# Kernel optimization log

Measured on AMD Instinct MI355X. Metric: run time of the kernel, lower is better.

## Reference

```python
import math
import jax, jax.numpy as jnp
import numpy as np

B, L, E, H, NL = 8, 512, 512, 8, 2


def setup_inputs() -> dict:
    key = jax.random.key(0)
    ks = jax.random.split(key, 12)
    s = 0.02  # weight init scale
    return {
        "inputs_4e": jax.random.normal(ks[0], (B, L, 4 * E), jnp.float32),
        "query_embed": jax.random.normal(ks[1], (B, L, E), jnp.float32),
        "rel": jax.random.normal(ks[2], (B, L, L), jnp.float32),
        "resp_rel": jax.random.normal(ks[3], (B, L, L), jnp.float32),
        "timestamp": jax.random.uniform(ks[4], (B, L, L), jnp.float32) * 10.0,
        "l1": jax.random.uniform(ks[5], (1,), jnp.float32),
        "l2": jax.random.uniform(ks[6], (1,), jnp.float32),
        "l3": jax.random.uniform(ks[7], (1,), jnp.float32),
        "Win": jax.random.normal(ks[8], (4 * E, E), jnp.float32) * s,
        "b_in": jnp.zeros((E,), jnp.float32),
        "Wqkv": jax.random.normal(ks[9], (NL, 3, E, E), jnp.float32) * s,
        "bqkv": jnp.zeros((NL, 3, E), jnp.float32),
        "Wf1": jax.random.normal(ks[10], (2 * E, E), jnp.float32) * s,
        "bf1": jnp.zeros((E,), jnp.float32),
        "Wf2": jax.random.normal(ks[11], (E, 1), jnp.float32) * s,
        "bf2": jnp.zeros((1,), jnp.float32),
    }


def _mha(q_in, k_in, v_in, Wq, bq, Wk, bk, Wv, bv,
         rel, resp_rel, timestamp, l1, l2, l3, mask):
    Bb, Ll, Ee = q_in.shape
    d = Ee // H

    def split(x, W, b):  # (B,L,E) -> (B,H,L,d)
        return (x @ W + b).reshape(Bb, Ll, H, d).transpose(0, 2, 1, 3)

    q = split(q_in, Wq, bq)
    k = split(k_in, Wk, bk)
    v = split(v_in, Wv, bv)

    # relation softmax: zero out where mask==False, -1e4 at zeros
    maskf = mask.astype(rel.dtype)              # (1,1,L,L)
    rel_m = rel[:, None, :, :] * maskf          # (B,1,L,L), broadcasts over heads
    rel_attn = jax.nn.softmax(jnp.where(rel_m == 0, -1e4, rel_m), axis=-1)
    resp_m = resp_rel[:, None, :, :] * maskf
    resp_attn = jax.nn.softmax(jnp.where(resp_m == 0, -1e4, resp_m), axis=-1)

    # QK softmax with causal mask
    scores = jnp.einsum('bhqd,bhkd->bhqk', q, k) / math.sqrt(d)
    scores = jnp.where(mask, -1e9, scores)
    prob_attn = jax.nn.softmax(scores, axis=-1)

    # time-decay softmax
    ts = jnp.exp(-jnp.abs(timestamp))[:, None, :, :]  # (B,1,L,L)
    ts = jnp.where(mask, -jnp.inf, ts)
    time_attn = jax.nn.softmax(ts, axis=-1)

    # blend (ablation flags all True)
    p = (1.0 - l2) * prob_attn + l2 * time_attn
    p = (1.0 - l1) * p + l1 * rel_attn
    p = (1.0 - l3) * p + l3 * resp_attn

    out = jnp.einsum('bhqk,bhkd->bhqd', p, v)
    out = out.transpose(0, 2, 1, 3).reshape(Bb, Ll, Ee)
    return out, p


def reference(inputs_4e, query_embed, rel, resp_rel, timestamp,
              l1, l2, l3, Win, b_in, Wqkv, bqkv, Wf1, bf1, Wf2, bf2):
    mask = jnp.triu(jnp.ones((1, 1, L, L), dtype=bool), k=1)  # future mask
    inputs = jax.nn.relu(inputs_4e @ Win + b_in)              # lin_in_interaction

    outputs, attn = _mha(query_embed, inputs, inputs,
                         Wqkv[0, 0], bqkv[0, 0], Wqkv[0, 1], bqkv[0, 1],
                         Wqkv[0, 2], bqkv[0, 2],
                         rel, resp_rel, timestamp, l1, l2, l3, mask)
    for i in range(1, NL):
        residual, attn = _mha(query_embed, outputs, outputs,
                              Wqkv[i, 0], bqkv[i, 0], Wqkv[i, 1], bqkv[i, 1],
                              Wqkv[i, 2], bqkv[i, 2],
                              rel, resp_rel, timestamp, l1, l2, l3, mask)
        outputs = outputs + jax.nn.relu(residual)

    concat_q = jnp.concatenate([outputs, query_embed], axis=-1)  # (B,L,2E)
    h = jax.nn.relu(concat_q @ Wf1 + bf1)
    return h @ Wf2 + bf2  # (B,L,1)
```

## Files before the change

kernel.cpp:

```cpp
#include <hip/hip_runtime.h>
#include <math.h>

namespace {
constexpr int B = 8, L = 512, E = 512, H = 8;
constexpr int M = B * L;
}

typedef float f32x4 __attribute__((ext_vector_type(4)));
typedef short bf16x8 __attribute__((ext_vector_type(8)));

__device__ inline ushort f2b(float f) {
  unsigned u = __float_as_uint(f);
  u += 0x7FFF + ((u >> 16) & 1);
  return (ushort)(u >> 16);
}
__device__ inline float b2f(ushort h) { return __uint_as_float(((unsigned)h) << 16); }

__device__ inline f32x4 mfma16(bf16x8 a, bf16x8 b, f32x4 c) {
  return __builtin_amdgcn_mfma_f32_16x16x32_bf16(a, b, c, 0, 0, 0);
}

__device__ __forceinline__ void gl2lds16(const ushort* g, ushort* l) {
  __builtin_amdgcn_global_load_lds(
      (const __attribute__((address_space(1))) void*)g,
      (__attribute__((address_space(3))) void*)l, 16, 0, 0);
}

template <int NROWS>
__device__ __forceinline__ void stage64(const ushort* __restrict__ g, int ldg,
                                        ushort* lds, int tid) {
  const int w = tid >> 6, l = tid & 63;
  constexpr int RPW = NROWS / 4;
  constexpr int NI = RPW / 8;
#pragma unroll
  for (int it = 0; it < NI; ++it) {
    const int rbase = w * RPW + it * 8;
    const int row = rbase + (l >> 3);
    const int chunk = (l & 7) ^ (row & 7);
    gl2lds16(g + (size_t)row * ldg + chunk * 8, lds + rbase * 64);
  }
}

template <int BM, int NBUF>
__device__ __forceinline__ void stage_comb(const ushort* b0, const ushort* b1,
                                           const ushort* b2, const ushort* b3,
                                           ushort* lds, int tid) {
#pragma unroll
  for (int it = 0; it < BM / 32; ++it) {
    const int row = (tid >> 3) + it * 32;
    const int slot = tid & 7;
    const size_t off = (size_t)row * 512 + slot * 8;
    union Uu { uint4 u; ushort s[8]; } va, vb, vc, vd, vo;
    va.u = *(const uint4*)(b0 + off);
    vb.u = *(const uint4*)(b1 + off);
    if (NBUF == 4) {
      vc.u = *(const uint4*)(b2 + off);
      vd.u = *(const uint4*)(b3 + off);
    }
#pragma unroll
    for (int e = 0; e < 8; ++e) {
      float f = b2f(va.s[e]) + b2f(vb.s[e]);
      if (NBUF == 4) f += fmaxf(b2f(vc.s[e]) + b2f(vd.s[e]), 0.f);
      vo.s[e] = f2b(f);
    }
    *(uint4*)(&lds[row * 64 + ((slot ^ (row & 7)) * 8)]) = vo.u;
  }
}

template <int BM, int MODE, int HAS_BIAS, int ACT, int STAGEA, int FUSE>
__device__ __forceinline__ void dev_gemm(
    ushort* lds, int bxx, int by, const ushort* A, const ushort* A2,
    const ushort* A3, const ushort* A4, const ushort* Aq,
    const ushort* Wt, const float* bias, ushort* C0, ushort* C1, ushort* C2,
    ushort* C3, const float* w2, float* outv, int K, int N) {
  ushort* Als = lds;
  ushort* Bls = lds + 2 * BM * 64;
  const int tid = threadIdx.x;
  const int l = tid & 63, wv = tid >> 6;
  const int wr = wv >> 1, wc = wv & 1;
  const int g = l >> 4, c = l & 15;
  constexpr int WM = BM / 2;
  constexpr int MFR = WM / 16;
  const int bm = by * BM;
  const int bn64 = bxx * 64;
  const int sec = (MODE == 3 || MODE == 5) ? (bn64 >> 9) : 0;
  const bool vsec = (MODE == 3 && sec == 2) || (MODE == 5 && sec == 1);

  const ushort* Ause = A;
  if (MODE == 3 && (sec == 1 || sec == 2)) Ause = A2;
  const int ldA = K;
  const ushort* Bp = Wt + (size_t)bn64 * K;

  f32x4 acc[MFR][2];
#pragma unroll
  for (int mi = 0; mi < MFR; ++mi)
#pragma unroll
    for (int ni = 0; ni < 2; ++ni) acc[mi][ni] = f32x4{0.f, 0.f, 0.f, 0.f};

  auto stageA = [&](int t, int buf) {
    ushort* dst = Als + buf * BM * 64;
    if (STAGEA == 0) {
      stage64<BM>(Ause + (size_t)bm * ldA + t * 64, ldA, dst, tid);
    } else if (STAGEA == 2) {
      stage_comb<BM, 2>(A + (size_t)bm * 512 + t * 64,
                        A2 + (size_t)bm * 512 + t * 64, nullptr, nullptr, dst, tid);
    } else {
      if (t < 8)
        stage_comb<BM, 4>(A + (size_t)bm * 512 + t * 64,
                          A2 + (size_t)bm * 512 + t * 64,
                          A3 + (size_t)bm * 512 + t * 64,
                          A4 + (size_t)bm * 512 + t * 64, dst, tid);
      else
        stage64<BM>(Aq + (size_t)bm * 512 + (t - 8) * 64, 512, dst, tid);
    }
  };

  stageA(0, 0);
  stage64<64>(Bp, K, Bls, tid);
  __syncthreads();

  const int NT = K >> 6;
  int cur = 0;
  for (int t = 0; t < NT; ++t) {
    if (t + 1 < NT) {
      stageA(t + 1, cur ^ 1);
      stage64<64>(Bp + (t + 1) * 64, K, Bls + (cur ^ 1) * 64 * 64, tid);
    }
#pragma unroll
    for (int ks = 0; ks < 2; ++ks) {
      bf16x8 af[MFR], bf_[2];
#pragma unroll
      for (int mi = 0; mi < MFR; ++mi) {
        const int row = wr * WM + mi * 16 + c;
        af[mi] = *(const bf16x8*)(&Als[cur * BM * 64 + row * 64 +
                                       (((ks * 4 + g) ^ (row & 7)) * 8)]);
      }
#pragma unroll
      for (int ni = 0; ni < 2; ++ni) {
        const int row = wc * 32 + ni * 16 + c;
        bf_[ni] = *(const bf16x8*)(&Bls[cur * 64 * 64 + row * 64 +
                                        (((ks * 4 + g) ^ (row & 7)) * 8)]);
      }
      if (vsec) {
#pragma unroll
        for (int mi = 0; mi < MFR; ++mi)
#pragma unroll
          for (int ni = 0; ni < 2; ++ni)
            acc[mi][ni] = mfma16(bf_[ni], af[mi], acc[mi][ni]);
      } else {
#pragma unroll
        for (int mi = 0; mi < MFR; ++mi)
#pragma unroll
          for (int ni = 0; ni < 2; ++ni)
            acc[mi][ni] = mfma16(af[mi], bf_[ni], acc[mi][ni]);
      }
    }
    __syncthreads();
    cur ^= 1;
  }

  if (FUSE) {
    float w2v[2];
#pragma unroll
    for (int ni = 0; ni < 2; ++ni) w2v[ni] = w2[bn64 + wc * 32 + ni * 16 + c];
#pragma unroll
    for (int mi = 0; mi < MFR; ++mi) {
#pragma unroll
      for (int r = 0; r < 4; ++r) {
        float p = 0.f;
#pragma unroll
        for (int ni = 0; ni < 2; ++ni) {
          const int n = bn64 + wc * 32 + ni * 16 + c;
          float v = acc[mi][ni][r] + bias[n];
          v = fmaxf(v, 0.f);
          p += v * w2v[ni];
        }
        p += __shfl_xor(p, 1);
        p += __shfl_xor(p, 2);
        p += __shfl_xor(p, 4);
        p += __shfl_xor(p, 8);
        if (c == 0) atomicAdd(&outv[bm + wr * WM + mi * 16 + g * 4 + r], p);
      }
    }
  } else if (vsec) {
    const int vbase = (MODE == 3) ? 1024 : 512;
    const int e0 = bn64 - vbase;
#pragma unroll
    for (int ni = 0; ni < 2; ++ni) {
#pragma unroll
      for (int r = 0; r < 4; ++r) {
        const int e = e0 + wc * 32 + ni * 16 + g * 4 + r;
        const float bv = HAS_BIAS ? bias[vbase + e] : 0.f;
#pragma unroll
        for (int mi = 0; mi < MFR; ++mi) {
          const int m = bm + wr * WM + mi * 16 + c;
          const int bb = m >> 9, lt = m & 511;
          C2[((size_t)bb * 512 + e) * 512 + lt] = f2b(acc[mi][ni][r] + bv);
        }
      }
    }
  } else {
    ushort* dst = C0;
    int nsub = 0, ldc = N;
    if (MODE == 3 || MODE == 5) {
      dst = (MODE == 5) ? C1 : (sec == 0 ? C0 : (sec == 1 ? C1 : C3));
      nsub = sec * 512;
      ldc = 512;
    }
#pragma unroll
    for (int ni = 0; ni < 2; ++ni) {
      const int n = bn64 + wc * 32 + ni * 16 + c;
      const float bv = HAS_BIAS ? bias[n] : 0.f;
#pragma unroll
      for (int mi = 0; mi < MFR; ++mi) {
#pragma unroll
        for (int r = 0; r < 4; ++r) {
          const int m = bm + wr * WM + mi * 16 + g * 4 + r;
          float v = acc[mi][ni][r] + bv;
          if (ACT) v = fmaxf(v, 0.f);
          dst[(size_t)m * ldc + (n - nsub)] = f2b(v);
        }
      }
    }
  }
}

__device__ __forceinline__ void dev_attn(ushort* lds, int bidx,
                                         const ushort* __restrict__ Qg,
                                         const ushort* __restrict__ Kg,
                                         const ushort* __restrict__ Vt,
                                         float c_p, ushort* __restrict__ aexp) {
  ushort* Qs = lds;
  ushort* Ps = lds + 4096;
  ushort* Ks = lds + 8192;
  ushort* Vs = lds + 16384;
  const int qt = 7 - (bidx & 7);
  const int h = (bidx >> 3) & 7;
  const int b = bidx >> 6;
  const int tid = threadIdx.x, l = tid & 63, w = tid >> 6;
  const int g = l >> 4, c = l & 15;
  const int qrow0 = b * L + qt * 64;
  const ushort* Kbase = Kg + (size_t)(b * L) * E + h * 64;
  const ushort* Vbase = Vt + (size_t)(b * E + h * 64) * L;

  stage64<64>(Qg + (size_t)qrow0 * E + h * 64, E, Qs, tid);
  stage64<64>(Kbase, E, Ks, tid);
  stage64<64>(Vbase, L, Vs, tid);
  __syncthreads();

  f32x4 o[4];
#pragma unroll
  for (int dn = 0; dn < 4; ++dn) o[dn] = f32x4{0.f, 0.f, 0.f, 0.f};
  float l_r[4] = {0.f, 0.f, 0.f, 0.f};

  int cur = 0;
  for (int kt = 0; kt <= qt; ++kt) {
    if (kt < qt) {
      stage64<64>(Kbase + (size_t)(kt + 1) * 64 * E, E, Ks + (cur ^ 1) * 4096, tid);
      stage64<64>(Vbase + (kt + 1) * 64, L, Vs + (cur ^ 1) * 4096, tid);
    }
    bf16x8 qf[2];
#pragma unroll
    for (int kq = 0; kq < 2; ++kq) {
      int row = w * 16 + c;
      qf[kq] = *(const bf16x8*)(&Qs[row * 64 + (((kq * 4 + g) ^ (row & 7)) * 8)]);
    }
    f32x4 s4[4];
#pragma unroll
    for (int n = 0; n < 4; ++n) s4[n] = f32x4{0.f, 0.f, 0.f, 0.f};
#pragma unroll
    for (int n = 0; n < 4; ++n) {
#pragma unroll
      for (int kq = 0; kq < 2; ++kq) {
        int row = n * 16 + c;
        bf16x8 kf = *(const bf16x8*)(&Ks[cur * 4096 + row * 64 +
                                         (((kq * 4 + g) ^ (row & 7)) * 8)]);
        s4[n] = mfma16(qf[kq], kf, s4[n]);
      }
    }
    const bool diag = (kt == qt);
    float pv[4][4];
    float lad[4] = {0.f, 0.f, 0.f, 0.f};
#pragma unroll
    for (int n = 0; n < 4; ++n)
#pragma unroll
      for (int r = 0; r < 4; ++r) {
        float sv = s4[n][r] * 0.125f;
        if (diag && (n * 16 + c) > (w * 16 + g * 4 + r)) sv = -1e30f;
        float p = __expf(sv);
        pv[n][r] = p;
        lad[r] += p;
      }
#pragma unroll
    for (int off = 1; off < 16; off <<= 1)
#pragma unroll
      for (int r = 0; r < 4; ++r) lad[r] += __shfl_xor(lad[r], off);
#pragma unroll
    for (int r = 0; r < 4; ++r) l_r[r] += lad[r];
#pragma unroll
    for (int n = 0; n < 4; ++n)
#pragma unroll
      for (int r = 0; r < 4; ++r) {
        int q = w * 16 + g * 4 + r;
        int byt = 32 * n + 2 * c;
        int slot = byt >> 4;
        Ps[q * 64 + ((slot ^ (q & 7)) * 8) + ((byt & 15) >> 1)] = f2b(pv[n][r]);
      }
    bf16x8 pf[2];
#pragma unroll
    for (int kq = 0; kq < 2; ++kq) {
      int row = w * 16 + c;
      pf[kq] = *(const bf16x8*)(&Ps[row * 64 + (((kq * 4 + g) ^ (row & 7)) * 8)]);
    }
#pragma unroll
    for (int dn = 0; dn < 4; ++dn) {
#pragma unroll
      for (int kq = 0; kq < 2; ++kq) {
        int row = dn * 16 + c;
        bf16x8 vf = *(const bf16x8*)(&Vs[cur * 4096 + row * 64 +
                                         (((kq * 4 + g) ^ (row & 7)) * 8)]);
        o[dn] = mfma16(pf[kq], vf, o[dn]);
      }
    }
    __syncthreads();
    cur ^= 1;
  }

  float linv[4];
#pragma unroll
  for (int r = 0; r < 4; ++r) linv[r] = c_p / l_r[r];
#pragma unroll
  for (int dn = 0; dn < 4; ++dn) {
#pragma unroll
    for (int r = 0; r < 4; ++r) {
      const size_t row = (size_t)qrow0 + w * 16 + g * 4 + r;
      const int col = h * 64 + dn * 16 + c;
      aexp[row * E + col] = f2b(o[dn][r] * linv[r]);
    }
  }
}

__device__ __forceinline__ void dev_blend(int idx, const float* __restrict__ rel,
                                          const float* __restrict__ resp,
                                          const float* __restrict__ ts,
                                          float l1, float l2, float l3,
                                          ushort* __restrict__ stat) {
  const float c_t = (1.f - l3) * (1.f - l1) * l2;
  const float c_r = (1.f - l3) * l1;
  const float c_s = l3;
  const int wave = threadIdx.x >> 6, lane = threadIdx.x & 63;
  const int row = idx * 4 + wave;
  const int qi = row & (L - 1);
  const size_t base = (size_t)row * L;
  float rv[8], sv[8], tv[8];
#pragma unroll
  for (int jj = 0; jj < 8; ++jj) {
    const int k = jj * 64 + lane;
    const float r = rel[base + k];
    const float s = resp[base + k];
    const float tt = ts[base + k];
    const bool fut = (k > qi);
    const float rm = fut ? r : 0.f;
    const float sm = fut ? s : 0.f;
    rv[jj] = (rm == 0.f) ? -1e4f : rm;
    sv[jj] = (sm == 0.f) ? -1e4f : sm;
    tv[jj] = fut ? -INFINITY : __expf(-fabsf(tt));
  }
  float rmax = -INFINITY, smax = -INFINITY, tmax = -INFINITY;
#pragma unroll
  for (int jj = 0; jj < 8; ++jj) {
    rmax = fmaxf(rmax, rv[jj]); smax = fmaxf(smax, sv[jj]); tmax = fmaxf(tmax, tv[jj]);
  }
  for (int off = 1; off < 64; off <<= 1) {
    rmax = fmaxf(rmax, __shfl_xor(rmax, off));
    smax = fmaxf(smax, __shfl_xor(smax, off));
    tmax = fmaxf(tmax, __shfl_xor(tmax, off));
  }
  float rsum = 0.f, ssum = 0.f, tsum = 0.f;
#pragma unroll
  for (int jj = 0; jj < 8; ++jj) {
    rsum += __expf(rv[jj] - rmax); ssum += __expf(sv[jj] - smax); tsum += __expf(tv[jj] - tmax);
  }
  for (int off = 1; off < 64; off <<= 1) {
    rsum += __shfl_xor(rsum, off);
    ssum += __shfl_xor(ssum, off);
    tsum += __shfl_xor(tsum, off);
  }
  const float rinv = c_r / rsum, sinv = c_s / ssum, tinv = c_t / tsum;
#pragma unroll
  for (int jj = 0; jj < 8; ++jj) {
    stat[base + jj * 64 + lane] =
        f2b(__expf(rv[jj] - rmax) * rinv + __expf(sv[jj] - smax) * sinv +
            __expf(tv[jj] - tmax) * tinv);
  }
}

__device__ __forceinline__ void tcvt_body(const float* __restrict__ src,
                                          ushort* __restrict__ dst, int Kd, int Nd,
                                          int kb, int nb, int t, ushort (*T)[33]) {
  const int r = t >> 3, c4 = (t & 7) * 4;
  float4 v = *(const float4*)(src + (size_t)(kb + r) * Nd + nb + c4);
  T[r][c4 + 0] = f2b(v.x); T[r][c4 + 1] = f2b(v.y);
  T[r][c4 + 2] = f2b(v.z); T[r][c4 + 3] = f2b(v.w);
  __syncthreads();
  ushort4 ov = {T[c4 + 0][r], T[c4 + 1][r], T[c4 + 2][r], T[c4 + 3][r]};
  *(ushort4*)(&dst[(size_t)(nb + r) * Kd + kb + c4]) = ov;
}

__global__ __launch_bounds__(256) void k_prep(
    const float* __restrict__ x4e, const float* __restrict__ query,
    const float* __restrict__ Win, const float* __restrict__ bf2,
    ushort* __restrict__ x4e_bf, ushort* __restrict__ qbf,
    ushort* __restrict__ Wint, float* __restrict__ outv) {
  __shared__ ushort T[32][33];
  const int NB_CVT = (M * 2048 / 4 + M * 512 / 4) / 256;
  const int bi = blockIdx.x;
  const int t = threadIdx.x;
  if (bi < NB_CVT) {
    const int N1 = M * 2048 / 4;
    int i = bi * 256 + t;
    if (i < N1) {
      float4 v = ((const float4*)x4e)[i];
      ushort4 o = {f2b(v.x), f2b(v.y), f2b(v.z), f2b(v.w)};
      ((ushort4*)x4e_bf)[i] = o;
    } else {
      int j = i - N1;
      float4 v = ((const float4*)query)[j];
      ushort4 o = {f2b(v.x), f2b(v.y), f2b(v.z), f2b(v.w)};
      ((ushort4*)qbf)[j] = o;
    }
    return;
  }
  if (bi < NB_CVT + 1024) {
    const int idx = bi - NB_CVT;
    tcvt_body(Win, Wint, 2048, 512, (idx >> 4) * 32, (idx & 15) * 32, t, T);
    return;
  }
  {
    const int i = (bi - NB_CVT - 1024) * 256 + t;
    const float b2 = bf2[0];
    float4 v = {b2, b2, b2, b2};
    ((float4*)outv)[i] = v;
  }
}

__global__ __launch_bounds__(256) void k_xgemm_blend(
    const ushort* __restrict__ x4e_bf, const ushort* __restrict__ Wint,
    const float* __restrict__ b_in, ushort* __restrict__ x_bf,
    const float* __restrict__ Wqkv, const float* __restrict__ Wf1,
    ushort* __restrict__ Wqkvt, ushort* __restrict__ Wf1t,
    const float* __restrict__ rel, const float* __restrict__ resp,
    const float* __restrict__ ts, const float* __restrict__ l1p,
    const float* __restrict__ l2p, const float* __restrict__ l3p,
    ushort* __restrict__ stat) {
  extern __shared__ ushort lds[];
  const int bx = blockIdx.x;
  if (bx < 512) {
    dev_gemm<64, 1, 1, 1, 0, 0>(lds, bx & 7, bx >> 3, x4e_bf, nullptr, nullptr,
                                nullptr, nullptr, Wint, b_in, x_bf, nullptr,
                                nullptr, nullptr, nullptr, nullptr, 2048, 512);
  } else if (bx < 2560) {
    const int idx = bx - 512;
    const long long EE = (long long)E * E;
    if (idx < 1536) {
      const int z = idx >> 8, r = idx & 255;
      tcvt_body(Wqkv + z * EE, Wqkvt + z * EE, 512, 512, (r >> 4) * 32,
                (r & 15) * 32, threadIdx.x, (ushort(*)[33])lds);
    } else {
      const int q = idx - 1536;
      tcvt_body(Wf1, Wf1t, 1024, 512, (q >> 4) * 32, (q & 15) * 32,
                threadIdx.x, (ushort(*)[33])lds);
    }
  } else {
    dev_blend(bx - 2560, rel, resp, ts, l1p[0], l2p[0], l3p[0], stat);
  }
}

__global__ __launch_bounds__(256) void k_qkv0(
    const ushort* __restrict__ query_bf, const ushort* __restrict__ x_bf,
    const ushort* __restrict__ Wqkvt, const float* __restrict__ bqkv,
    ushort* __restrict__ q_bf, ushort* __restrict__ k_bf,
    ushort* __restrict__ vt, ushort* __restrict__ q1_bf) {
  extern __shared__ ushort lds[];
  dev_gemm<128, 3, 1, 0, 0, 0>(lds, blockIdx.x, blockIdx.y, query_bf, x_bf,
                               nullptr, nullptr, nullptr, Wqkvt, bqkv, q_bf,
                               k_bf, vt, q1_bf, nullptr, nullptr, 512, 2048);
}

__global__ __launch_bounds__(256) void k_attn_stat(
    const ushort* __restrict__ Qg, const ushort* __restrict__ Kg,
    const ushort* __restrict__ Vt, const ushort* __restrict__ stat,
    const float* __restrict__ l1p, const float* __restrict__ l2p,
    const float* __restrict__ l3p, ushort* __restrict__ aexp,
    ushort* __restrict__ ostat) {
  extern __shared__ ushort lds[];
  const int bx = blockIdx.x;
  if (bx < 512) {
    const float l1 = l1p[0], l2 = l2p[0], l3 = l3p[0];
    const float c_p = (1.f - l3) * (1.f - l1) * (1.f - l2);
    dev_attn(lds, bx, Qg, Kg, Vt, c_p, aexp);
  } else {
    const int idx = bx - 512;
    const int bz = idx >> 6, r = idx & 63;
    const long long LLs = (long long)L * L, ELs = (long long)E * L;
    dev_gemm<64, 1, 0, 0, 0, 0>(lds, r & 7, r >> 3, stat + bz * LLs, nullptr,
                                nullptr, nullptr, nullptr, Vt + bz * ELs,
                                nullptr, ostat + bz * ELs, nullptr, nullptr,
                                nullptr, nullptr, nullptr, 512, 512);
  }
}

__global__ __launch_bounds__(256) void k_kv1(
    const ushort* __restrict__ aexp0, const ushort* __restrict__ ostat0,
    const ushort* __restrict__ Wt, const float* __restrict__ bias,
    ushort* __restrict__ k_bf, ushort* __restrict__ vt) {
  extern __shared__ ushort lds[];
  dev_gemm<128, 5, 1, 0, 2, 0>(lds, blockIdx.x, blockIdx.y, aexp0, ostat0,
                               nullptr, nullptr, nullptr, Wt, bias, nullptr,
                               k_bf, vt, nullptr, nullptr, nullptr, 512, 1024);
}

__global__ __launch_bounds__(256) void k_f1(
    const ushort* __restrict__ aexp0, const ushort* __restrict__ ostat0,
    const ushort* __restrict__ aexp1, const ushort* __restrict__ ostat1,
    const ushort* __restrict__ query_bf, const ushort* __restrict__ Wf1t,
    const float* __restrict__ bf1, const float* __restrict__ Wf2,
    float* __restrict__ outv) {
  extern __shared__ ushort lds[];
  dev_gemm<64, 4, 1, 1, 4, 1>(lds, blockIdx.x, blockIdx.y, aexp0, ostat0,
                              aexp1, ostat1, query_bf, Wf1t, bf1, nullptr,
                              nullptr, nullptr, nullptr, Wf2, outv, 1024, 512);
}

extern "C" void kernel_launch(void* const* d_in, const int* in_sizes, int n_in,
                              void* d_out, int out_size, void* d_ws, size_t ws_size,
                              hipStream_t stream) {
  (void)in_sizes; (void)n_in; (void)out_size; (void)ws_size;
  const float* inputs_4e = (const float*)d_in[0];
  const float* query = (const float*)d_in[1];
  const float* rel = (const float*)d_in[2];
  const float* resp = (const float*)d_in[3];
  const float* tsp = (const float*)d_in[4];
  const float* l1p = (const float*)d_in[5];
  const float* l2p = (const float*)d_in[6];
  const float* l3p = (const float*)d_in[7];
  const float* Win = (const float*)d_in[8];
  const float* b_in = (const float*)d_in[9];
  const float* Wqkv = (const float*)d_in[10];
  const float* bqkv = (const float*)d_in[11];
  const float* Wf1 = (const float*)d_in[12];
  const float* bf1 = (const float*)d_in[13];
  const float* Wf2 = (const float*)d_in[14];
  const float* bf2 = (const float*)d_in[15];

  char* ws = (char*)d_ws;
  const size_t MB = 1ull << 20;
  ushort* x4e_bf  = (ushort*)(ws + 0 * MB);
  ushort* aexp0   = (ushort*)(ws + 0 * MB);
  ushort* ostat0  = (ushort*)(ws + 4 * MB);
  ushort* aexp1   = (ushort*)(ws + 8 * MB);
  ushort* ostat1  = (ushort*)(ws + 12 * MB);
  ushort* query_bf= (ushort*)(ws + 16 * MB);
  ushort* stat_bf = (ushort*)(ws + 20 * MB);
  ushort* x_bf    = (ushort*)(ws + 24 * MB);
  ushort* q_bf    = (ushort*)(ws + 28 * MB);
  ushort* k_bf    = (ushort*)(ws + 32 * MB);
  ushort* vt      = (ushort*)(ws + 36 * MB);
  ushort* q1_bf   = (ushort*)(ws + 40 * MB);
  ushort* Wint    = (ushort*)(ws + 48 * MB);
  ushort* Wqkvt   = (ushort*)(ws + 50 * MB);
  ushort* Wf1t    = (ushort*)(ws + 53 * MB);

  const long long EE = (long long)E * E;
  const int LDS_G64 = (2 * 64 * 64 + 2 * 64 * 64) * 2;
  const int LDS_G128 = (2 * 128 * 64 + 2 * 64 * 64) * 2;
  const int LDS_AS = 49152;

  k_prep<<<10240 + 1024 + 4, 256, 0, stream>>>(inputs_4e, query, Win, bf2,
                                               x4e_bf, query_bf, Wint,
                                               (float*)d_out);
  k_xgemm_blend<<<512 + 2048 + 1024, 256, LDS_G64, stream>>>(
      x4e_bf, Wint, b_in, x_bf, Wqkv, Wf1, Wqkvt, Wf1t,
      rel, resp, tsp, l1p, l2p, l3p, stat_bf);
  k_qkv0<<<dim3(32, 32), 256, LDS_G128, stream>>>(query_bf, x_bf, Wqkvt, bqkv,
                                                  q_bf, k_bf, vt, q1_bf);
  k_attn_stat<<<1024, 256, LDS_AS, stream>>>(q_bf, k_bf, vt, stat_bf,
                                             l1p, l2p, l3p, aexp0, ostat0);
  k_kv1<<<dim3(16, 32), 256, LDS_G128, stream>>>(aexp0, ostat0, Wqkvt + 4 * EE,
                                                 bqkv + 4 * E, k_bf, vt);
  k_attn_stat<<<1024, 256, LDS_AS, stream>>>(q1_bf, k_bf, vt, stat_bf,
                                             l1p, l2p, l3p, aexp1, ostat1);
  k_f1<<<dim3(8, 64), 256, LDS_G64, stream>>>(aexp0, ostat0, aexp1, ostat1,
                                              query_bf, Wf1t, bf1, Wf2,
                                              (float*)d_out);
}
```

Measured before the change: 141.3 us.

## Move query projections into earlier kernel and enlarge GEMM tiles to 128 rows

The Q and Q1 projections of the query embedding now run inside the x-GEMM/blend kernel, since they depend only on the query, and the Wq weight transposes move into the prep kernel. The old combined QKV0 kernel becomes a K/V-only GEMM, which takes work off the critical chain. Several GEMMs switch from 64-row to 128-row tiles and launch fewer blocks. The conversion blocks in the prep kernel each process four chunks. The larger tiles reduce the number of blocks and may lower occupancy or load balance.

```diff
diff --git a/kernel.cpp b/kernel.cpp
--- a/kernel.cpp
+++ b/kernel.cpp
@@ -72,7 +72,7 @@
     ushort* lds, int bxx, int by, const ushort* A, const ushort* A2,
     const ushort* A3, const ushort* A4, const ushort* Aq,
     const ushort* Wt, const float* bias, ushort* C0, ushort* C1, ushort* C2,
-    ushort* C3, const float* w2, float* outv, int K, int N) {
+    const float* w2, float* outv, int K, int N) {
   ushort* Als = lds;
   ushort* Bls = lds + 2 * BM * 64;
   const int tid = threadIdx.x;
@@ -83,11 +83,10 @@
   constexpr int MFR = WM / 16;
   const int bm = by * BM;
   const int bn64 = bxx * 64;
-  const int sec = (MODE == 3 || MODE == 5) ? (bn64 >> 9) : 0;
-  const bool vsec = (MODE == 3 && sec == 2) || (MODE == 5 && sec == 1);
-
-  const ushort* Ause = A;
-  if (MODE == 3 && (sec == 1 || sec == 2)) Ause = A2;
+  const int sec = (MODE == 5) ? (bn64 >> 9) : 0;
+  const bool vsec = (MODE == 5 && sec == 1);
+
+  const ushort* Ause = (MODE == 5) ? A2 : A;
   const int ldA = K;
   const ushort* Bp = Wt + (size_t)bn64 * K;
 
@@ -183,14 +182,13 @@
       }
     }
   } else if (vsec) {
-    const int vbase = (MODE == 3) ? 1024 : 512;
-    const int e0 = bn64 - vbase;
+    const int e0 = bn64 - 512;
 #pragma unroll
     for (int ni = 0; ni < 2; ++ni) {
 #pragma unroll
       for (int r = 0; r < 4; ++r) {
         const int e = e0 + wc * 32 + ni * 16 + g * 4 + r;
-        const float bv = HAS_BIAS ? bias[vbase + e] : 0.f;
+        const float bv = HAS_BIAS ? bias[512 + e] : 0.f;
 #pragma unroll
         for (int mi = 0; mi < MFR; ++mi) {
           const int m = bm + wr * WM + mi * 16 + c;
@@ -200,13 +198,9 @@
       }
     }
   } else {
-    ushort* dst = C0;
-    int nsub = 0, ldc = N;
-    if (MODE == 3 || MODE == 5) {
-      dst = (MODE == 5) ? C1 : (sec == 0 ? C0 : (sec == 1 ? C1 : C3));
-      nsub = sec * 512;
-      ldc = 512;
-    }
+    ushort* dst = (MODE == 5) ? C1 : C0;
+    const int nsub = (MODE == 5) ? sec * 512 : 0;
+    const int ldc = (MODE == 5) ? 512 : N;
 #pragma unroll
     for (int ni = 0; ni < 2; ++ni) {
       const int n = bn64 + wc * 32 + ni * 16 + c;
@@ -409,35 +403,47 @@
 
 __global__ __launch_bounds__(256) void k_prep(
     const float* __restrict__ x4e, const float* __restrict__ query,
-    const float* __restrict__ Win, const float* __restrict__ bf2,
-    ushort* __restrict__ x4e_bf, ushort* __restrict__ qbf,
-    ushort* __restrict__ Wint, float* __restrict__ outv) {
+    const float* __restrict__ Win, const float* __restrict__ Wqkv,
+    const float* __restrict__ bf2, ushort* __restrict__ x4e_bf,
+    ushort* __restrict__ qbf, ushort* __restrict__ Wint,
+    ushort* __restrict__ Wqkvt, float* __restrict__ outv) {
   __shared__ ushort T[32][33];
-  const int NB_CVT = (M * 2048 / 4 + M * 512 / 4) / 256;
   const int bi = blockIdx.x;
   const int t = threadIdx.x;
-  if (bi < NB_CVT) {
+  const long long EE = (long long)E * E;
+  if (bi < 2560) {
     const int N1 = M * 2048 / 4;
-    int i = bi * 256 + t;
-    if (i < N1) {
-      float4 v = ((const float4*)x4e)[i];
-      ushort4 o = {f2b(v.x), f2b(v.y), f2b(v.z), f2b(v.w)};
-      ((ushort4*)x4e_bf)[i] = o;
-    } else {
-      int j = i - N1;
-      float4 v = ((const float4*)query)[j];
-      ushort4 o = {f2b(v.x), f2b(v.y), f2b(v.z), f2b(v.w)};
-      ((ushort4*)qbf)[j] = o;
+#pragma unroll
+    for (int it = 0; it < 4; ++it) {
+      int i = bi * 1024 + it * 256 + t;
+      if (i < N1) {
+        float4 v = ((const float4*)x4e)[i];
+        ushort4 o = {f2b(v.x), f2b(v.y), f2b(v.z), f2b(v.w)};
+        ((ushort4*)x4e_bf)[i] = o;
+      } else {
+        int j = i - N1;
+        float4 v = ((const float4*)query)[j];
+        ushort4 o = {f2b(v.x), f2b(v.y), f2b(v.z), f2b(v.w)};
+        ((ushort4*)qbf)[j] = o;
+      }
     }
     return;
   }
-  if (bi < NB_CVT + 1024) {
-    const int idx = bi - NB_CVT;
+  if (bi < 3584) {
+    const int idx = bi - 2560;
     tcvt_body(Win, Wint, 2048, 512, (idx >> 4) * 32, (idx & 15) * 32, t, T);
     return;
   }
+  if (bi < 4096) {
+    const int idx = bi - 3584;
+    const int z = (idx >= 256) ? 3 : 0;
+    const int r = idx & 255;
+    tcvt_body(Wqkv + z * EE, Wqkvt + z * EE, 512, 512, (r >> 4) * 32,
+              (r & 15) * 32, t, T);
+    return;
+  }
   {
-    const int i = (bi - NB_CVT - 1024) * 256 + t;
+    const int i = (bi - 4096) * 256 + t;
     const float b2 = bf2[0];
     float4 v = {b2, b2, b2, b2};
     ((float4*)outv)[i] = v;
@@ -445,46 +451,57 @@
 }
 
 __global__ __launch_bounds__(256) void k_xgemm_blend(
-    const ushort* __restrict__ x4e_bf, const ushort* __restrict__ Wint,
-    const float* __restrict__ b_in, ushort* __restrict__ x_bf,
-    const float* __restrict__ Wqkv, const float* __restrict__ Wf1,
-    ushort* __restrict__ Wqkvt, ushort* __restrict__ Wf1t,
-    const float* __restrict__ rel, const float* __restrict__ resp,
-    const float* __restrict__ ts, const float* __restrict__ l1p,
-    const float* __restrict__ l2p, const float* __restrict__ l3p,
-    ushort* __restrict__ stat) {
+    const ushort* __restrict__ x4e_bf, const ushort* __restrict__ query_bf,
+    const ushort* __restrict__ Wint, const ushort* __restrict__ Wqkvt,
+    const float* __restrict__ b_in, const float* __restrict__ bqkv,
+    ushort* __restrict__ x_bf, ushort* __restrict__ q_bf,
+    ushort* __restrict__ q1_bf, const float* __restrict__ Wqkv,
+    const float* __restrict__ Wf1, ushort* __restrict__ Wqkvt_out,
+    ushort* __restrict__ Wf1t, const float* __restrict__ rel,
+    const float* __restrict__ resp, const float* __restrict__ ts,
+    const float* __restrict__ l1p, const float* __restrict__ l2p,
+    const float* __restrict__ l3p, ushort* __restrict__ stat) {
   extern __shared__ ushort lds[];
   const int bx = blockIdx.x;
-  if (bx < 512) {
-    dev_gemm<64, 1, 1, 1, 0, 0>(lds, bx & 7, bx >> 3, x4e_bf, nullptr, nullptr,
-                                nullptr, nullptr, Wint, b_in, x_bf, nullptr,
-                                nullptr, nullptr, nullptr, nullptr, 2048, 512);
-  } else if (bx < 2560) {
-    const int idx = bx - 512;
-    const long long EE = (long long)E * E;
-    if (idx < 1536) {
-      const int z = idx >> 8, r = idx & 255;
-      tcvt_body(Wqkv + z * EE, Wqkvt + z * EE, 512, 512, (r >> 4) * 32,
-                (r & 15) * 32, threadIdx.x, (ushort(*)[33])lds);
-    } else {
-      const int q = idx - 1536;
-      tcvt_body(Wf1, Wf1t, 1024, 512, (q >> 4) * 32, (q & 15) * 32,
-                threadIdx.x, (ushort(*)[33])lds);
-    }
+  const long long EE = (long long)E * E;
+  if (bx < 256) {
+    dev_gemm<128, 1, 1, 1, 0, 0>(lds, bx & 7, bx >> 3, x4e_bf, nullptr, nullptr,
+                                 nullptr, nullptr, Wint, b_in, x_bf, nullptr,
+                                 nullptr, nullptr, nullptr, 2048, 512);
+  } else if (bx < 512) {
+    const int r = bx - 256;
+    dev_gemm<128, 1, 1, 0, 0, 0>(lds, r & 7, r >> 3, query_bf, nullptr, nullptr,
+                                 nullptr, nullptr, Wqkvt, bqkv, q_bf, nullptr,
+                                 nullptr, nullptr, nullptr, 512, 512);
+  } else if (bx < 768) {
+    const int r = bx - 512;
+    dev_gemm<128, 1, 1, 0, 0, 0>(lds, r & 7, r >> 3, query_bf, nullptr, nullptr,
+                                 nullptr, nullptr, Wqkvt + 3 * EE, bqkv + 3 * E,
+                                 q1_bf, nullptr, nullptr, nullptr, nullptr, 512, 512);
+  } else if (bx < 1792) {
+    const int idx = bx - 768;
+    const int zmap[4] = {1, 2, 4, 5};
+    const int z = zmap[idx >> 8];
+    const int r = idx & 255;
+    tcvt_body(Wqkv + z * EE, Wqkvt_out + z * EE, 512, 512, (r >> 4) * 32,
+              (r & 15) * 32, threadIdx.x, (ushort(*)[33])lds);
+  } else if (bx < 2304) {
+    const int q = bx - 1792;
+    tcvt_body(Wf1, Wf1t, 1024, 512, (q >> 4) * 32, (q & 15) * 32,
+              threadIdx.x, (ushort(*)[33])lds);
   } else {
-    dev_blend(bx - 2560, rel, resp, ts, l1p[0], l2p[0], l3p[0], stat);
-  }
-}
-
-__global__ __launch_bounds__(256) void k_qkv0(
-    const ushort* __restrict__ query_bf, const ushort* __restrict__ x_bf,
-    const ushort* __restrict__ Wqkvt, const float* __restrict__ bqkv,
-    ushort* __restrict__ q_bf, ushort* __restrict__ k_bf,
-    ushort* __restrict__ vt, ushort* __restrict__ q1_bf) {
+    dev_blend(bx - 2304, rel, resp, ts, l1p[0], l2p[0], l3p[0], stat);
+  }
+}
+
+__global__ __launch_bounds__(256) void k_kv0(
+    const ushort* __restrict__ x_bf, const ushort* __restrict__ Wt,
+    const float* __restrict__ bias, ushort* __restrict__ k_bf,
+    ushort* __restrict__ vt) {
   extern __shared__ ushort lds[];
-  dev_gemm<128, 3, 1, 0, 0, 0>(lds, blockIdx.x, blockIdx.y, query_bf, x_bf,
-                               nullptr, nullptr, nullptr, Wqkvt, bqkv, q_bf,
-                               k_bf, vt, q1_bf, nullptr, nullptr, 512, 2048);
+  dev_gemm<128, 5, 1, 0, 0, 0>(lds, blockIdx.x, blockIdx.y, nullptr, x_bf,
+                               nullptr, nullptr, nullptr, Wt, bias, nullptr,
+                               k_bf, vt, nullptr, nullptr, 512, 1024);
 }
 
 __global__ __launch_bounds__(256) void k_attn_stat(
@@ -501,12 +518,12 @@
     dev_attn(lds, bx, Qg, Kg, Vt, c_p, aexp);
   } else {
     const int idx = bx - 512;
-    const int bz = idx >> 6, r = idx & 63;
+    const int bz = idx >> 5, r = idx & 31;
     const long long LLs = (long long)L * L, ELs = (long long)E * L;
-    dev_gemm<64, 1, 0, 0, 0, 0>(lds, r & 7, r >> 3, stat + bz * LLs, nullptr,
-                                nullptr, nullptr, nullptr, Vt + bz * ELs,
-                                nullptr, ostat + bz * ELs, nullptr, nullptr,
-                                nullptr, nullptr, nullptr, 512, 512);
+    dev_gemm<128, 1, 0, 0, 0, 0>(lds, r & 7, r >> 3, stat + bz * LLs, nullptr,
+                                 nullptr, nullptr, nullptr, Vt + bz * ELs,
+                                 nullptr, ostat + bz * ELs, nullptr, nullptr,
+                                 nullptr, nullptr, 512, 512);
   }
 }
 
@@ -517,7 +534,7 @@
   extern __shared__ ushort lds[];
   dev_gemm<128, 5, 1, 0, 2, 0>(lds, blockIdx.x, blockIdx.y, aexp0, ostat0,
                                nullptr, nullptr, nullptr, Wt, bias, nullptr,
-                               k_bf, vt, nullptr, nullptr, nullptr, 512, 1024);
+                               k_bf, vt, nullptr, nullptr, 512, 1024);
 }
 
 __global__ __launch_bounds__(256) void k_f1(
@@ -527,9 +544,9 @@
     const float* __restrict__ bf1, const float* __restrict__ Wf2,
     float* __restrict__ outv) {
   extern __shared__ ushort lds[];
-  dev_gemm<64, 4, 1, 1, 4, 1>(lds, blockIdx.x, blockIdx.y, aexp0, ostat0,
-                              aexp1, ostat1, query_bf, Wf1t, bf1, nullptr,
-                              nullptr, nullptr, nullptr, Wf2, outv, 1024, 512);
+  dev_gemm<128, 4, 1, 1, 4, 1>(lds, blockIdx.x, blockIdx.y, aexp0, ostat0,
+                               aexp1, ostat1, query_bf, Wf1t, bf1, nullptr,
+                               nullptr, nullptr, Wf2, outv, 1024, 512);
 }
 
 extern "C" void kernel_launch(void* const* d_in, const int* in_sizes, int n_in,
@@ -572,25 +589,24 @@
   ushort* Wf1t    = (ushort*)(ws + 53 * MB);
 
   const long long EE = (long long)E * E;
-  const int LDS_G64 = (2 * 64 * 64 + 2 * 64 * 64) * 2;
   const int LDS_G128 = (2 * 128 * 64 + 2 * 64 * 64) * 2;
   const int LDS_AS = 49152;
 
-  k_prep<<<10240 + 1024 + 4, 256, 0, stream>>>(inputs_4e, query, Win, bf2,
-                                               x4e_bf, query_bf, Wint,
-                                               (float*)d_out);
-  k_xgemm_blend<<<512 + 2048 + 1024, 256, LDS_G64, stream>>>(
-      x4e_bf, Wint, b_in, x_bf, Wqkv, Wf1, Wqkvt, Wf1t,
-      rel, resp, tsp, l1p, l2p, l3p, stat_bf);
-  k_qkv0<<<dim3(32, 32), 256, LDS_G128, stream>>>(query_bf, x_bf, Wqkvt, bqkv,
-                                                  q_bf, k_bf, vt, q1_bf);
-  k_attn_stat<<<1024, 256, LDS_AS, stream>>>(q_bf, k_bf, vt, stat_bf,
-                                             l1p, l2p, l3p, aexp0, ostat0);
+  k_prep<<<2560 + 1024 + 512 + 4, 256, 0, stream>>>(
+      inputs_4e, query, Win, Wqkv, bf2, x4e_bf, query_bf, Wint, Wqkvt,
+      (float*)d_out);
+  k_xgemm_blend<<<256 + 512 + 1024 + 512 + 1024, 256, LDS_G128, stream>>>(
+      x4e_bf, query_bf, Wint, Wqkvt, b_in, bqkv, x_bf, q_bf, q1_bf,
+      Wqkv, Wf1, Wqkvt, Wf1t, rel, resp, tsp, l1p, l2p, l3p, stat_bf);
+  k_kv0<<<dim3(16, 32), 256, LDS_G128, stream>>>(x_bf, Wqkvt + 1 * EE,
+                                                 bqkv + 1 * E, k_bf, vt);
+  k_attn_stat<<<768, 256, LDS_AS, stream>>>(q_bf, k_bf, vt, stat_bf,
+                                            l1p, l2p, l3p, aexp0, ostat0);
   k_kv1<<<dim3(16, 32), 256, LDS_G128, stream>>>(aexp0, ostat0, Wqkvt + 4 * EE,
                                                  bqkv + 4 * E, k_bf, vt);
-  k_attn_stat<<<1024, 256, LDS_AS, stream>>>(q1_bf, k_bf, vt, stat_bf,
-                                             l1p, l2p, l3p, aexp1, ostat1);
-  k_f1<<<dim3(8, 64), 256, LDS_G64, stream>>>(aexp0, ostat0, aexp1, ostat1,
-                                              query_bf, Wf1t, bf1, Wf2,
-                                              (float*)d_out);
-}
+  k_attn_stat<<<768, 256, LDS_AS, stream>>>(q1_bf, k_bf, vt, stat_bf,
+                                            l1p, l2p, l3p, aexp1, ostat1);
+  k_f1<<<dim3(8, 32), 256, LDS_G128, stream>>>(aexp0, ostat0, aexp1, ostat1,
+                                               query_bf, Wf1t, bf1, Wf2,
+                                               (float*)d_out);
+}
```

Result: no change. 140.9 us (-0.3%).
